# Kernel tuning notes

Hardware: AMD Instinct MI355X
Metric: run time of the kernel (lower is better)

The kernel has to match this reference:

```python
import jax, jax.numpy as jnp
import numpy as np

B, H, W, D = 4, 256, 256, 128  # batch, height, width, channels (dim)
PAD = 1  # mask_padding -> band half-width


def setup_inputs() -> dict:
    key = jax.random.key(0)
    ks = jax.random.split(key, 6)
    s = 0.05  # weight init scale
    return {
        "x": jax.random.normal(ks[0], (B, H, W, D), jnp.float32),
        "kv": jax.random.normal(ks[1], (B, H, W, D), jnp.float32),
        "Wq_h": jax.random.normal(ks[2], (D, D), jnp.float32) * s,
        "Wk_h": jax.random.normal(ks[3], (D, D), jnp.float32) * s,
        "Wq_w": jax.random.normal(ks[4], (D, D), jnp.float32) * s,
        "Wk_w": jax.random.normal(ks[5], (D, D), jnp.float32) * s,
    }


def _band_mask(t, pad, dtype):
    # Equivalent to conv2d(identity, horizontal-line kernel): 1 where |i-j| <= pad
    i = jnp.arange(t)
    return (jnp.abs(i[:, None] - i[None, :]) <= pad).astype(dtype)


def _attend(xa, kva, Wq, Wk, pad):
    # xa, kva: [N, t, d]; heads==1 so dim_heads == d (per source early-return quirk)
    q = xa @ Wq.T                                   # [N, t, d]
    k = kva @ Wk.T                                  # [N, t, d]
    e = q.shape[-1]
    dots = jnp.einsum('bie,bje->bij', q, k) * (e ** -0.5)  # [N, t, t]
    mask = _band_mask(dots.shape[-1], pad, dots.dtype)
    dots = dots + (1.0 - mask) * (-30000.0)
    attn = jax.nn.softmax(dots, axis=-1)
    # NOTE: original multiplies attention weights with raw kv (not v projection)
    return jnp.einsum('bij,bjd->bid', attn, kva)    # [N, t, d]


def reference(x, kv, Wq_h, Wk_h, Wq_w, Wk_w):
    b, h, w, d = x.shape
    # Axis 1 (height): permutation [0,2,1,3]
    xh = jnp.transpose(x, (0, 2, 1, 3)).reshape(b * w, h, d)
    kvh = jnp.transpose(kv, (0, 2, 1, 3)).reshape(b * w, h, d)
    oh = _attend(xh, kvh, Wq_h, Wk_h, PAD).reshape(b, w, h, d)
    oh = jnp.transpose(oh, (0, 2, 1, 3))
    # Axis 2 (width): identity permutation [0,1,2,3]
    xw = x.reshape(b * h, w, d)
    kvw = kv.reshape(b * h, w, d)
    ow = _attend(xw, kvw, Wq_w, Wk_w, PAD).reshape(b, h, w, d)
    return oh + ow  # sum_axial_out=True
```

## Files before the change

### kernel.cpp

```cpp
#include <hip/hip_runtime.h>

#define DD    128
#define LINE  256
#define NPOS  262144
#define BP    32
#define TILE  64
#define NROW  66
#define NROWP 80
#define LSTR  136

typedef __bf16 bf16x8 __attribute__((ext_vector_type(8)));
typedef float  f32x4v __attribute__((ext_vector_type(4)));
typedef float  f32x2v __attribute__((ext_vector_type(2)));
typedef unsigned int u32x2v __attribute__((ext_vector_type(2)));
typedef unsigned int u32x4v __attribute__((ext_vector_type(4)));

static __device__ __forceinline__ unsigned short f2bf(float f) {
  union { float f; unsigned u; } v; v.f = f;
  unsigned u = v.u + 0x7FFFu + ((v.u >> 16) & 1u);
  return (unsigned short)(u >> 16);
}
#define BF_LO(u) __uint_as_float((u) << 16)
#define BF_HI(u) __uint_as_float((u) & 0xffff0000u)


__global__ void make_mt_kernel(const float* __restrict__ Wq_h, const float* __restrict__ Wk_h,
                               const float* __restrict__ Wq_w, const float* __restrict__ Wk_w,
                               unsigned short* __restrict__ Ms) {
  const float* Wq = blockIdx.y ? Wq_w : Wq_h;
  const float* Wk = blockIdx.y ? Wk_w : Wk_h;
  unsigned short* M = Ms + blockIdx.y * (DD * DD);
  int d = blockIdx.x, c = threadIdx.x;
  float acc = 0.f;
  for (int e = 0; e < DD; ++e) acc += Wq[e * DD + c] * Wk[e * DD + d];
  M[d * DD + c] = f2bf(acc * 0.08838834764831845f);
}

static __device__ __forceinline__ float dot8(const float q[8], f32x4v a, f32x4v b) {
  return q[0] * a.x + q[1] * a.y + q[2] * a.z + q[3] * a.w
       + q[4] * b.x + q[5] * b.y + q[6] * b.z + q[7] * b.w;
}
static __device__ __forceinline__ float red16(float v) {
#pragma unroll
  for (int m = 1; m < 16; m <<= 1) v += __shfl_xor(v, m, 16);
  return v;
}
static __device__ __forceinline__ void dec4(unsigned lo, unsigned hi, float* q) {
  q[0] = BF_LO(lo); q[1] = BF_HI(lo); q[2] = BF_LO(hi); q[3] = BF_HI(hi);
}

__global__ __launch_bounds__(256) void fused_kernel(const float* __restrict__ x,
                                                    const float* __restrict__ kv,
                                                    const unsigned short* __restrict__ Mt,
                                                    float* __restrict__ out) {
  __shared__ unsigned short x_s[BP * LSTR];
  __shared__ unsigned short xm_s[2 * BP * LSTR];

  const int tid = threadIdx.x;
  const int y  = blockIdx.y;
  const int h  = y & 255;
  const int w0 = blockIdx.x * BP;
  const long row0 = (long)y * 256 + w0;

  for (int u = tid; u < BP * 32; u += 256) {
    int row = u >> 5, c4 = u & 31;
    f32x4v v = *(const f32x4v*)(x + (row0 + row) * DD + c4 * 4);
    u32x2v wv;
    wv.x = (unsigned)f2bf(v.x) | ((unsigned)f2bf(v.y) << 16);
    wv.y = (unsigned)f2bf(v.z) | ((unsigned)f2bf(v.w) << 16);
    *(u32x2v*)&x_s[row * LSTR + c4 * 4] = wv;
  }
  __syncthreads();

  {
    const int wave = tid >> 6, lane = tid & 63;
    const int r16 = lane & 15, q = lane >> 4;
    const unsigned short* Mm = Mt + (wave >> 1) * (DD * DD);
    unsigned short* XO = xm_s + (wave >> 1) * (BP * LSTR);
#pragma unroll
    for (int ci = 0; ci < 4; ++ci) {
      int ct = (wave & 1) * 4 + ci;
      bf16x8 b[4];
#pragma unroll
      for (int ks = 0; ks < 4; ++ks)
        b[ks] = __builtin_bit_cast(
            bf16x8, *(const u32x4v*)(Mm + (ct * 16 + r16) * DD + ks * 32 + q * 8));
#pragma unroll
      for (int rt = 0; rt < BP / 16; ++rt) {
        f32x4v acc = {0.f, 0.f, 0.f, 0.f};
#pragma unroll
        for (int ks = 0; ks < 4; ++ks) {
          bf16x8 a = __builtin_bit_cast(
              bf16x8, *(const u32x4v*)&x_s[(rt * 16 + r16) * LSTR + ks * 32 + q * 8]);
          acc = __builtin_amdgcn_mfma_f32_16x16x32_bf16(a, b[ks], acc, 0, 0, 0);
        }
#pragma unroll
        for (int r = 0; r < 4; ++r) {
          int row = rt * 16 + q * 4 + r;
          XO[row * LSTR + ct * 16 + r16] = f2bf(acc[r]);
        }
      }
    }
  }
  __syncthreads();

  for (int it = 0; it < BP / 16; ++it) {
    const int g = it * 16 + (tid >> 4), l = tid & 15;
    const int w = w0 + g;
    const long pos = row0 + g;
    const long pn = (h > 0)   ? pos - 256 : pos;
    const long ps = (h < 255) ? pos + 256 : pos;
    const long pw = (w > 0)   ? pos - 1   : pos;
    const long pe = (w < 255) ? pos + 1   : pos;
    const int c0 = l * 4, c1 = 64 + l * 4;

    f32x4v cA = *(const f32x4v*)(kv + pos * DD + c0);
    f32x4v cB = *(const f32x4v*)(kv + pos * DD + c1);
    f32x4v nA = *(const f32x4v*)(kv + pn * DD + c0);
    f32x4v nB = *(const f32x4v*)(kv + pn * DD + c1);
    f32x4v sA = *(const f32x4v*)(kv + ps * DD + c0);
    f32x4v sB = *(const f32x4v*)(kv + ps * DD + c1);
    f32x4v wA = *(const f32x4v*)(kv + pw * DD + c0);
    f32x4v wB = *(const f32x4v*)(kv + pw * DD + c1);
    f32x4v eA = *(const f32x4v*)(kv + pe * DD + c0);
    f32x4v eB = *(const f32x4v*)(kv + pe * DD + c1);

    u32x2v xh0 = *(const u32x2v*)&xm_s[g * LSTR + c0];
    u32x2v xh1 = *(const u32x2v*)&xm_s[g * LSTR + c1];
    u32x2v xw0 = *(const u32x2v*)&xm_s[BP * LSTR + g * LSTR + c0];
    u32x2v xw1 = *(const u32x2v*)&xm_s[BP * LSTR + g * LSTR + c1];
    float qh[8], qw[8];
    dec4(xh0.x, xh0.y, qh); dec4(xh1.x, xh1.y, qh + 4);
    dec4(xw0.x, xw0.y, qw); dec4(xw1.x, xw1.y, qw + 4);

    float sh_n = red16(dot8(qh, nA, nB));
    float sh_c = red16(dot8(qh, cA, cB));
    float sh_s = red16(dot8(qh, sA, sB));
    float sw_w = red16(dot8(qw, wA, wB));
    float sw_c = red16(dot8(qw, cA, cB));
    float sw_e = red16(dot8(qw, eA, eB));

    if (h == 0)   sh_n = -1e30f;
    if (h == 255) sh_s = -1e30f;
    if (w == 0)   sw_w = -1e30f;
    if (w == 255) sw_e = -1e30f;

    float mh = fmaxf(sh_n, fmaxf(sh_c, sh_s));
    float e0 = __expf(sh_n - mh), e1 = __expf(sh_c - mh), e2 = __expf(sh_s - mh);
    float ih = 1.f / (e0 + e1 + e2);
    float ph0 = e0 * ih, ph1 = e1 * ih, ph2 = e2 * ih;

    float mw = fmaxf(sw_w, fmaxf(sw_c, sw_e));
    float f0 = __expf(sw_w - mw), f1 = __expf(sw_c - mw), f2 = __expf(sw_e - mw);
    float iw = 1.f / (f0 + f1 + f2);
    float pw0 = f0 * iw, pw1 = f1 * iw, pw2 = f2 * iw;

    float pc = ph1 + pw1;
    f32x4v oA, oB;
    oA.x = ph0 * nA.x + pc * cA.x + ph2 * sA.x + pw0 * wA.x + pw2 * eA.x;
    oA.y = ph0 * nA.y + pc * cA.y + ph2 * sA.y + pw0 * wA.y + pw2 * eA.y;
    oA.z = ph0 * nA.z + pc * cA.z + ph2 * sA.z + pw0 * wA.z + pw2 * eA.z;
    oA.w = ph0 * nA.w + pc * cA.w + ph2 * sA.w + pw0 * wA.w + pw2 * eA.w;
    oB.x = ph0 * nB.x + pc * cB.x + ph2 * sB.x + pw0 * wB.x + pw2 * eB.x;
    oB.y = ph0 * nB.y + pc * cB.y + ph2 * sB.y + pw0 * wB.y + pw2 * eB.y;
    oB.z = ph0 * nB.z + pc * cB.z + ph2 * sB.z + pw0 * wB.z + pw2 * eB.z;
    oB.w = ph0 * nB.w + pc * cB.w + ph2 * sB.w + pw0 * wB.w + pw2 * eB.w;
    *(f32x4v*)(out + pos * DD + c0) = oA;
    *(f32x4v*)(out + pos * DD + c1) = oB;
  }
}

__global__ void make_m_kernel(const float* __restrict__ Wq_h, const float* __restrict__ Wk_h,
                              const float* __restrict__ Wq_w, const float* __restrict__ Wk_w,
                              unsigned short* __restrict__ Ms) {
  const float* Wq = blockIdx.y ? Wq_w : Wq_h;
  const float* Wk = blockIdx.y ? Wk_w : Wk_h;
  unsigned short* M = Ms + blockIdx.y * (DD * DD);
  int d = blockIdx.x, c = threadIdx.x;
  float acc = 0.f;
  for (int e = 0; e < DD; ++e) acc += Wq[e * DD + d] * Wk[e * DD + c];
  M[d * DD + c] = f2bf(acc * 0.08838834764831845f);
}

template <int AXIS, bool ADD>
__global__ __launch_bounds__(256) void axial_pass(const float* __restrict__ x,
                                                  const float* __restrict__ kv,
                                                  const unsigned short* __restrict__ M,
                                                  float* __restrict__ out) {
  __shared__ unsigned short kv_s[NROWP * LSTR];
  __shared__ unsigned short x_s[TILE * LSTR];
  __shared__ unsigned short kvm_s[NROW * LSTR];
  __shared__ float s_s[3 * TILE];
  __shared__ float p_s[3 * TILE];

  const int tid  = threadIdx.x;
  const int seg0 = blockIdx.x * TILE;
  const int line = blockIdx.y;

  size_t base; int stride;
  if (AXIS == 0) {
    int b = line >> 8, w = line & 255;
    base = (size_t)b * (256 * 256 * 128) + (size_t)w * DD;
    stride = 256 * 128;
  } else {
    base = (size_t)line * (256 * 128);
    stride = DD;
  }

  for (int u = tid; u < NROWP * 32; u += 256) {
    int row = u >> 5, c4 = u & 31;
    u32x2v wv; wv.x = 0u; wv.y = 0u;
    if (row < NROW) {
      int pos = seg0 - 1 + row;
      pos = pos < 0 ? 0 : (pos > LINE - 1 ? LINE - 1 : pos);
      f32x4v v = *(const f32x4v*)(kv + base + (size_t)pos * stride + c4 * 4);
      wv.x = (unsigned)f2bf(v.x) | ((unsigned)f2bf(v.y) << 16);
      wv.y = (unsigned)f2bf(v.z) | ((unsigned)f2bf(v.w) << 16);
    }
    *(u32x2v*)&kv_s[row * LSTR + c4 * 4] = wv;
  }
  for (int u = tid; u < TILE * 32; u += 256) {
    int row = u >> 5, c4 = u & 31;
    f32x4v v = *(const f32x4v*)(x + base + (size_t)(seg0 + row) * stride + c4 * 4);
    u32x2v wv;
    wv.x = (unsigned)f2bf(v.x) | ((unsigned)f2bf(v.y) << 16);
    wv.y = (unsigned)f2bf(v.z) | ((unsigned)f2bf(v.w) << 16);
    *(u32x2v*)&x_s[row * LSTR + c4 * 4] = wv;
  }
  __syncthreads();

  {
    const int wave = tid >> 6, lane = tid & 63;
    const int r16 = lane & 15, q = lane >> 4;
    for (int ct = wave * 2; ct < wave * 2 + 2; ++ct) {
      bf16x8 b[4];
#pragma unroll
      for (int ks = 0; ks < 4; ++ks)
        b[ks] = __builtin_bit_cast(
            bf16x8, *(const u32x4v*)(M + (ct * 16 + r16) * DD + ks * 32 + q * 8));
#pragma unroll
      for (int rt = 0; rt < 5; ++rt) {
        f32x4v acc = {0.f, 0.f, 0.f, 0.f};
#pragma unroll
        for (int ks = 0; ks < 4; ++ks) {
          bf16x8 a = __builtin_bit_cast(
              bf16x8, *(const u32x4v*)&kv_s[(rt * 16 + r16) * LSTR + ks * 32 + q * 8]);
          acc = __builtin_amdgcn_mfma_f32_16x16x32_bf16(a, b[ks], acc, 0, 0, 0);
        }
        int col = ct * 16 + r16;
#pragma unroll
        for (int r = 0; r < 4; ++r) {
          int row = rt * 16 + q * 4 + r;
          if (row < NROW) kvm_s[row * LSTR + col] = f2bf(acc[r]);
        }
      }
    }
  }
  __syncthreads();

  {
    int i = tid >> 2, sub = tid & 3;
    float s0 = 0.f, s1 = 0.f, s2 = 0.f;
#pragma unroll
    for (int ch = 0; ch < 4; ++ch) {
      int off = sub * 32 + ch * 8;
      float xf[8];
      {
        u32x4v t = *(const u32x4v*)&x_s[i * LSTR + off];
        xf[0] = BF_LO(t.x); xf[1] = BF_HI(t.x); xf[2] = BF_LO(t.y); xf[3] = BF_HI(t.y);
        xf[4] = BF_LO(t.z); xf[5] = BF_HI(t.z); xf[6] = BF_LO(t.w); xf[7] = BF_HI(t.w);
      }
      {
        u32x4v t = *(const u32x4v*)&kvm_s[(i + 0) * LSTR + off];
        s0 += xf[0]*BF_LO(t.x) + xf[1]*BF_HI(t.x) + xf[2]*BF_LO(t.y) + xf[3]*BF_HI(t.y)
            + xf[4]*BF_LO(t.z) + xf[5]*BF_HI(t.z) + xf[6]*BF_LO(t.w) + xf[7]*BF_HI(t.w);
      }
      {
        u32x4v t = *(const u32x4v*)&kvm_s[(i + 1) * LSTR + off];
        s1 += xf[0]*BF_LO(t.x) + xf[1]*BF_HI(t.x) + xf[2]*BF_LO(t.y) + xf[3]*BF_HI(t.y)
            + xf[4]*BF_LO(t.z) + xf[5]*BF_HI(t.z) + xf[6]*BF_LO(t.w) + xf[7]*BF_HI(t.w);
      }
      {
        u32x4v t = *(const u32x4v*)&kvm_s[(i + 2) * LSTR + off];
        s2 += xf[0]*BF_LO(t.x) + xf[1]*BF_HI(t.x) + xf[2]*BF_LO(t.y) + xf[3]*BF_HI(t.y)
            + xf[4]*BF_LO(t.z) + xf[5]*BF_HI(t.z) + xf[6]*BF_LO(t.w) + xf[7]*BF_HI(t.w);
      }
    }
    s0 += __shfl_xor(s0, 1); s0 += __shfl_xor(s0, 2);
    s1 += __shfl_xor(s1, 1); s1 += __shfl_xor(s1, 2);
    s2 += __shfl_xor(s2, 1); s2 += __shfl_xor(s2, 2);
    if (sub == 0) {
      int gp = seg0 + i;
      s_s[0 * TILE + i] = (gp - 1 >= 0)   ? s0 : -1e30f;
      s_s[1 * TILE + i] = s1;
      s_s[2 * TILE + i] = (gp + 1 < LINE) ? s2 : -1e30f;
    }
  }
  __syncthreads();

  if (tid < TILE) {
    float s0 = s_s[0 * TILE + tid], s1 = s_s[1 * TILE + tid], s2 = s_s[2 * TILE + tid];
    float m = fmaxf(s0, fmaxf(s1, s2));
    float e0 = __expf(s0 - m), e1 = __expf(s1 - m), e2 = __expf(s2 - m);
    float inv = 1.f / (e0 + e1 + e2);
    p_s[0 * TILE + tid] = e0 * inv;
    p_s[1 * TILE + tid] = e1 * inv;
    p_s[2 * TILE + tid] = e2 * inv;
  }
  __syncthreads();

  for (int r = 0; r < 16; ++r) {
    int u  = r * 256 + tid;
    int i  = u >> 6, dp = u & 63;
    float p0 = p_s[0 * TILE + i], p1 = p_s[1 * TILE + i], p2 = p_s[2 * TILE + i];
    unsigned a0 = *(const unsigned*)&kv_s[(i + 0) * LSTR + dp * 2];
    unsigned a1 = *(const unsigned*)&kv_s[(i + 1) * LSTR + dp * 2];
    unsigned a2 = *(const unsigned*)&kv_s[(i + 2) * LSTR + dp * 2];
    f32x2v o;
    o.x = p0 * BF_LO(a0) + p1 * BF_LO(a1) + p2 * BF_LO(a2);
    o.y = p0 * BF_HI(a0) + p1 * BF_HI(a1) + p2 * BF_HI(a2);
    size_t oidx = base + (size_t)(seg0 + i) * stride + dp * 2;
    if (ADD) {
      f32x2v prev = *(const f32x2v*)(out + oidx);
      o.x += prev.x; o.y += prev.y;
    }
    *(f32x2v*)(out + oidx) = o;
  }
}

extern "C" void kernel_launch(void* const* d_in, const int* in_sizes, int n_in,
                              void* d_out, int out_size, void* d_ws, size_t ws_size,
                              hipStream_t stream) {
  const float* x    = (const float*)d_in[0];
  const float* kv   = (const float*)d_in[1];
  const float* Wq_h = (const float*)d_in[2];
  const float* Wk_h = (const float*)d_in[3];
  const float* Wq_w = (const float*)d_in[4];
  const float* Wk_w = (const float*)d_in[5];
  float* out = (float*)d_out;

  const size_t ms_bytes = 2ull * DD * DD * 2;

  if (ws_size >= ms_bytes) {
    unsigned short* Ms = (unsigned short*)d_ws;
    make_mt_kernel<<<dim3(DD, 2), dim3(DD), 0, stream>>>(Wq_h, Wk_h, Wq_w, Wk_w, Ms);
    fused_kernel<<<dim3(LINE / BP, 4 * LINE), dim3(256), 0, stream>>>(x, kv, Ms, out);
  } else {
    unsigned short* Ms = (unsigned short*)d_ws;
    make_m_kernel<<<dim3(DD, 2), dim3(DD), 0, stream>>>(Wq_h, Wk_h, Wq_w, Wk_w, Ms);
    dim3 grid(LINE / TILE, 4 * 256);
    axial_pass<0, false><<<grid, dim3(256), 0, stream>>>(x, kv, Ms, out);
    axial_pass<1, true ><<<grid, dim3(256), 0, stream>>>(x, kv, Ms + DD * DD, out);
  }
}
```

Before: 359.5 us.

## Load x directly into MFMA registers, re-read kv neighbors to cut register pressure

Removes the x staging buffer in shared memory by loading x straight from global memory into MFMA A-operand registers, with a hardware bf16 conversion. The GEMM loop order is swapped so A stays in registers and B is streamed. In the attention stage the kv neighbor vectors are no longer held live across the softmax; they are re-read from global/L2 for the output sum. Launch bounds request 8 blocks per CU. Together these aim at higher occupancy through lower LDS and register use, at the cost of duplicate kv loads and possibly less coalesced x reads.

```diff
diff --git a/kernel.cpp b/kernel.cpp
--- a/kernel.cpp
+++ b/kernel.cpp
@@ -19,6 +19,12 @@
   union { float f; unsigned u; } v; v.f = f;
   unsigned u = v.u + 0x7FFFu + ((v.u >> 16) & 1u);
   return (unsigned short)(u >> 16);
+}
+static __device__ __forceinline__ unsigned pkbf(float a, float b) {
+  __bf16 x = (__bf16)a, y = (__bf16)b;
+  unsigned short ux = __builtin_bit_cast(unsigned short, x);
+  unsigned short uy = __builtin_bit_cast(unsigned short, y);
+  return (unsigned)ux | ((unsigned)uy << 16);
 }
 #define BF_LO(u) __uint_as_float((u) << 16)
 #define BF_HI(u) __uint_as_float((u) & 0xffff0000u)
@@ -49,11 +55,10 @@
   q[0] = BF_LO(lo); q[1] = BF_HI(lo); q[2] = BF_LO(hi); q[3] = BF_HI(hi);
 }
 
-__global__ __launch_bounds__(256) void fused_kernel(const float* __restrict__ x,
-                                                    const float* __restrict__ kv,
-                                                    const unsigned short* __restrict__ Mt,
-                                                    float* __restrict__ out) {
-  __shared__ unsigned short x_s[BP * LSTR];
+__global__ __launch_bounds__(256, 8) void fused_kernel(const float* __restrict__ x,
+                                                       const float* __restrict__ kv,
+                                                       const unsigned short* __restrict__ Mt,
+                                                       float* __restrict__ out) {
   __shared__ unsigned short xm_s[2 * BP * LSTR];
 
   const int tid = threadIdx.x;
@@ -62,37 +67,33 @@
   const int w0 = blockIdx.x * BP;
   const long row0 = (long)y * 256 + w0;
 
-  for (int u = tid; u < BP * 32; u += 256) {
-    int row = u >> 5, c4 = u & 31;
-    f32x4v v = *(const f32x4v*)(x + (row0 + row) * DD + c4 * 4);
-    u32x2v wv;
-    wv.x = (unsigned)f2bf(v.x) | ((unsigned)f2bf(v.y) << 16);
-    wv.y = (unsigned)f2bf(v.z) | ((unsigned)f2bf(v.w) << 16);
-    *(u32x2v*)&x_s[row * LSTR + c4 * 4] = wv;
-  }
-  __syncthreads();
-
   {
     const int wave = tid >> 6, lane = tid & 63;
     const int r16 = lane & 15, q = lane >> 4;
     const unsigned short* Mm = Mt + (wave >> 1) * (DD * DD);
     unsigned short* XO = xm_s + (wave >> 1) * (BP * LSTR);
 #pragma unroll
-    for (int ci = 0; ci < 4; ++ci) {
-      int ct = (wave & 1) * 4 + ci;
-      bf16x8 b[4];
-#pragma unroll
-      for (int ks = 0; ks < 4; ++ks)
-        b[ks] = __builtin_bit_cast(
-            bf16x8, *(const u32x4v*)(Mm + (ct * 16 + r16) * DD + ks * 32 + q * 8));
-#pragma unroll
-      for (int rt = 0; rt < BP / 16; ++rt) {
+    for (int rt = 0; rt < BP / 16; ++rt) {
+      bf16x8 a[4];
+#pragma unroll
+      for (int ks = 0; ks < 4; ++ks) {
+        const float* xp = x + (row0 + rt * 16 + r16) * DD + ks * 32 + q * 8;
+        f32x4v v0 = *(const f32x4v*)xp;
+        f32x4v v1 = *(const f32x4v*)(xp + 4);
+        u32x4v pk;
+        pk.x = pkbf(v0.x, v0.y); pk.y = pkbf(v0.z, v0.w);
+        pk.z = pkbf(v1.x, v1.y); pk.w = pkbf(v1.z, v1.w);
+        a[ks] = __builtin_bit_cast(bf16x8, pk);
+      }
+#pragma unroll
+      for (int ci = 0; ci < 4; ++ci) {
+        int ct = (wave & 1) * 4 + ci;
         f32x4v acc = {0.f, 0.f, 0.f, 0.f};
 #pragma unroll
         for (int ks = 0; ks < 4; ++ks) {
-          bf16x8 a = __builtin_bit_cast(
-              bf16x8, *(const u32x4v*)&x_s[(rt * 16 + r16) * LSTR + ks * 32 + q * 8]);
-          acc = __builtin_amdgcn_mfma_f32_16x16x32_bf16(a, b[ks], acc, 0, 0, 0);
+          bf16x8 b = __builtin_bit_cast(
+              bf16x8, *(const u32x4v*)(Mm + (ct * 16 + r16) * DD + ks * 32 + q * 8));
+          acc = __builtin_amdgcn_mfma_f32_16x16x32_bf16(a[ks], b, acc, 0, 0, 0);
         }
 #pragma unroll
         for (int r = 0; r < 4; ++r) {
@@ -113,17 +114,11 @@
     const long pw = (w > 0)   ? pos - 1   : pos;
     const long pe = (w < 255) ? pos + 1   : pos;
     const int c0 = l * 4, c1 = 64 + l * 4;
-
-    f32x4v cA = *(const f32x4v*)(kv + pos * DD + c0);
-    f32x4v cB = *(const f32x4v*)(kv + pos * DD + c1);
-    f32x4v nA = *(const f32x4v*)(kv + pn * DD + c0);
-    f32x4v nB = *(const f32x4v*)(kv + pn * DD + c1);
-    f32x4v sA = *(const f32x4v*)(kv + ps * DD + c0);
-    f32x4v sB = *(const f32x4v*)(kv + ps * DD + c1);
-    f32x4v wA = *(const f32x4v*)(kv + pw * DD + c0);
-    f32x4v wB = *(const f32x4v*)(kv + pw * DD + c1);
-    f32x4v eA = *(const f32x4v*)(kv + pe * DD + c0);
-    f32x4v eB = *(const f32x4v*)(kv + pe * DD + c1);
+    const float* kc = kv + pos * DD;
+    const float* kn = kv + pn * DD;
+    const float* ksr = kv + ps * DD;
+    const float* kw = kv + pw * DD;
+    const float* ke = kv + pe * DD;
 
     u32x2v xh0 = *(const u32x2v*)&xm_s[g * LSTR + c0];
     u32x2v xh1 = *(const u32x2v*)&xm_s[g * LSTR + c1];
@@ -133,12 +128,22 @@
     dec4(xh0.x, xh0.y, qh); dec4(xh1.x, xh1.y, qh + 4);
     dec4(xw0.x, xw0.y, qw); dec4(xw1.x, xw1.y, qw + 4);
 
-    float sh_n = red16(dot8(qh, nA, nB));
-    float sh_c = red16(dot8(qh, cA, cB));
-    float sh_s = red16(dot8(qh, sA, sB));
-    float sw_w = red16(dot8(qw, wA, wB));
-    float sw_c = red16(dot8(qw, cA, cB));
-    float sw_e = red16(dot8(qw, eA, eB));
+    float sh_n, sh_c, sh_s, sw_w, sw_c, sw_e;
+    {
+      f32x4v a, b;
+      a = *(const f32x4v*)(kn + c0);  b = *(const f32x4v*)(kn + c1);
+      sh_n = dot8(qh, a, b);
+      a = *(const f32x4v*)(kc + c0);  b = *(const f32x4v*)(kc + c1);
+      sh_c = dot8(qh, a, b); sw_c = dot8(qw, a, b);
+      a = *(const f32x4v*)(ksr + c0); b = *(const f32x4v*)(ksr + c1);
+      sh_s = dot8(qh, a, b);
+      a = *(const f32x4v*)(kw + c0);  b = *(const f32x4v*)(kw + c1);
+      sw_w = dot8(qw, a, b);
+      a = *(const f32x4v*)(ke + c0);  b = *(const f32x4v*)(ke + c1);
+      sw_e = dot8(qw, a, b);
+    }
+    sh_n = red16(sh_n); sh_c = red16(sh_c); sh_s = red16(sh_s);
+    sw_w = red16(sw_w); sw_c = red16(sw_c); sw_e = red16(sw_e);
 
     if (h == 0)   sh_n = -1e30f;
     if (h == 255) sh_s = -1e30f;
@@ -154,17 +159,27 @@
     float f0 = __expf(sw_w - mw), f1 = __expf(sw_c - mw), f2 = __expf(sw_e - mw);
     float iw = 1.f / (f0 + f1 + f2);
     float pw0 = f0 * iw, pw1 = f1 * iw, pw2 = f2 * iw;
-
     float pc = ph1 + pw1;
+
     f32x4v oA, oB;
-    oA.x = ph0 * nA.x + pc * cA.x + ph2 * sA.x + pw0 * wA.x + pw2 * eA.x;
-    oA.y = ph0 * nA.y + pc * cA.y + ph2 * sA.y + pw0 * wA.y + pw2 * eA.y;
-    oA.z = ph0 * nA.z + pc * cA.z + ph2 * sA.z + pw0 * wA.z + pw2 * eA.z;
-    oA.w = ph0 * nA.w + pc * cA.w + ph2 * sA.w + pw0 * wA.w + pw2 * eA.w;
-    oB.x = ph0 * nB.x + pc * cB.x + ph2 * sB.x + pw0 * wB.x + pw2 * eB.x;
-    oB.y = ph0 * nB.y + pc * cB.y + ph2 * sB.y + pw0 * wB.y + pw2 * eB.y;
-    oB.z = ph0 * nB.z + pc * cB.z + ph2 * sB.z + pw0 * wB.z + pw2 * eB.z;
-    oB.w = ph0 * nB.w + pc * cB.w + ph2 * sB.w + pw0 * wB.w + pw2 * eB.w;
+    {
+      f32x4v a, b;
+      a = *(const f32x4v*)(kc + c0);  b = *(const f32x4v*)(kc + c1);
+      oA.x = pc * a.x; oA.y = pc * a.y; oA.z = pc * a.z; oA.w = pc * a.w;
+      oB.x = pc * b.x; oB.y = pc * b.y; oB.z = pc * b.z; oB.w = pc * b.w;
+      a = *(const f32x4v*)(kn + c0);  b = *(const f32x4v*)(kn + c1);
+      oA.x += ph0 * a.x; oA.y += ph0 * a.y; oA.z += ph0 * a.z; oA.w += ph0 * a.w;
+      oB.x += ph0 * b.x; oB.y += ph0 * b.y; oB.z += ph0 * b.z; oB.w += ph0 * b.w;
+      a = *(const f32x4v*)(ksr + c0); b = *(const f32x4v*)(ksr + c1);
+      oA.x += ph2 * a.x; oA.y += ph2 * a.y; oA.z += ph2 * a.z; oA.w += ph2 * a.w;
+      oB.x += ph2 * b.x; oB.y += ph2 * b.y; oB.z += ph2 * b.z; oB.w += ph2 * b.w;
+      a = *(const f32x4v*)(kw + c0);  b = *(const f32x4v*)(kw + c1);
+      oA.x += pw0 * a.x; oA.y += pw0 * a.y; oA.z += pw0 * a.z; oA.w += pw0 * a.w;
+      oB.x += pw0 * b.x; oB.y += pw0 * b.y; oB.z += pw0 * b.z; oB.w += pw0 * b.w;
+      a = *(const f32x4v*)(ke + c0);  b = *(const f32x4v*)(ke + c1);
+      oA.x += pw2 * a.x; oA.y += pw2 * a.y; oA.z += pw2 * a.z; oA.w += pw2 * a.w;
+      oB.x += pw2 * b.x; oB.y += pw2 * b.y; oB.z += pw2 * b.z; oB.w += pw2 * b.w;
+    }
     *(f32x4v*)(out + pos * DD + c0) = oA;
     *(f32x4v*)(out + pos * DD + c1) = oB;
   }
```

New measurement: 461.1 us. 28.3% more time.
